# Kernel tuning notes

Hardware: AMD Instinct MI355X
Metric: run time of the kernel (lower is better)

The kernel has to match this reference:

```python
import jax, jax.numpy as jnp
import numpy as np

B, IN, OUT = 8192, 4096, 4096

def setup_inputs() -> dict:
    key = jax.random.key(0)
    ks = jax.random.split(key, 7)
    # sigma params initialized near -3 as in the torch module
    return {
        "x": jax.random.normal(ks[0], (B, IN), dtype=jnp.float32),
        "weight_mu": 0.1 * jax.random.normal(ks[1], (OUT, IN), dtype=jnp.float32),
        "weight_sigma": -3.0 + 0.1 * jax.random.normal(ks[2], (OUT, IN), dtype=jnp.float32),
        "bias_mu": 0.1 * jax.random.normal(ks[3], (OUT,), dtype=jnp.float32),
        "bias_sigma": -3.0 + 0.1 * jax.random.normal(ks[4], (OUT,), dtype=jnp.float32),
        "eps_w": jax.random.normal(ks[5], (OUT, IN), dtype=jnp.float32),
        "eps_b": jax.random.normal(ks[6], (OUT,), dtype=jnp.float32),
    }

def reference(x, weight_mu, weight_sigma, bias_mu, bias_sigma, eps_w, eps_b):
    # Reparameterized sample: w = mu + exp(sigma) * eps
    weight = weight_mu + jnp.exp(weight_sigma) * eps_w          # [OUT, IN]
    bias = bias_mu + jnp.exp(bias_sigma) * eps_b                # [OUT]
    out = jnp.einsum('bi,oi->bo', x, weight) + bias             # [B, OUT]
    # KL(q || N(0,1)); note log(var) == 2*sigma
    weight_var = jnp.exp(2.0 * weight_sigma)
    bias_var = jnp.exp(2.0 * bias_sigma)
    kl_w = -0.5 * jnp.sum(1.0 + 2.0 * weight_sigma - weight_mu ** 2 - weight_var)
    kl_b = -0.5 * jnp.sum(1.0 + 2.0 * bias_sigma - bias_mu ** 2 - bias_var)
    return out, kl_w + kl_b
```

## Files before the change

kernel.cpp:

```cpp
#include <hip/hip_runtime.h>

#define MDIM 8192
#define NDIM 4096
#define KDIM 4096
#define BK 32

typedef unsigned short u16;
typedef __attribute__((ext_vector_type(8))) short short8;
typedef __attribute__((ext_vector_type(4))) float f32x4;

__device__ __forceinline__ u16 f2b(float f) {
  unsigned u = __float_as_uint(f);
  u += 0x7FFFu + ((u >> 16) & 1u);
  return (u16)(u >> 16);
}
__device__ __forceinline__ unsigned pk2(float a, float b) {
  return (unsigned)f2b(a) | ((unsigned)f2b(b) << 16);
}

__device__ __forceinline__ void async16(const u16* g, u16* l) {
  __builtin_amdgcn_global_load_lds(
      (const __attribute__((address_space(1))) unsigned*)g,
      (__attribute__((address_space(3))) unsigned*)l, 16, 0, 0);
}

__global__ __launch_bounds__(256) void k_prep(const float4* __restrict__ wmu,
                                              const float4* __restrict__ wsg,
                                              const float4* __restrict__ wep,
                                              uint4* __restrict__ wb,
                                              const float4* __restrict__ x,
                                              uint4* __restrict__ xb,
                                              float* __restrict__ partials) {
  const int bx = blockIdx.x;
  if (bx < 8192) {
    const int i = bx * 256 + (int)threadIdx.x;
    float part = 0.f;
    uint4 o;
    {
      float4 m = wmu[2 * i], s = wsg[2 * i], e = wep[2 * i];
      float e0 = __expf(s.x), e1 = __expf(s.y), e2 = __expf(s.z), e3 = __expf(s.w);
      o.x = pk2(m.x + e0 * e.x, m.y + e1 * e.y);
      o.y = pk2(m.z + e2 * e.z, m.w + e3 * e.w);
      part += (1.f + 2.f * s.x - m.x * m.x - e0 * e0)
            + (1.f + 2.f * s.y - m.y * m.y - e1 * e1)
            + (1.f + 2.f * s.z - m.z * m.z - e2 * e2)
            + (1.f + 2.f * s.w - m.w * m.w - e3 * e3);
    }
    {
      float4 m = wmu[2 * i + 1], s = wsg[2 * i + 1], e = wep[2 * i + 1];
      float e0 = __expf(s.x), e1 = __expf(s.y), e2 = __expf(s.z), e3 = __expf(s.w);
      o.z = pk2(m.x + e0 * e.x, m.y + e1 * e.y);
      o.w = pk2(m.z + e2 * e.z, m.w + e3 * e.w);
      part += (1.f + 2.f * s.x - m.x * m.x - e0 * e0)
            + (1.f + 2.f * s.y - m.y * m.y - e1 * e1)
            + (1.f + 2.f * s.z - m.z * m.z - e2 * e2)
            + (1.f + 2.f * s.w - m.w * m.w - e3 * e3);
    }
    wb[i] = o;
    for (int off = 32; off; off >>= 1) part += __shfl_down(part, off, 64);
    __shared__ float red[4];
    const int lane = threadIdx.x & 63, wv = threadIdx.x >> 6;
    if (lane == 0) red[wv] = part;
    __syncthreads();
    if (threadIdx.x == 0)
      partials[bx] = red[0] + red[1] + red[2] + red[3];
  } else {
    const int i0 = (bx - 8192) * 256 + (int)threadIdx.x;
#pragma unroll
    for (int c = 0; c < 2; ++c) {
      const int i = i0 + c * (8192 * 256);
      float4 a = x[2 * i], b = x[2 * i + 1];
      uint4 o;
      o.x = pk2(a.x, a.y); o.y = pk2(a.z, a.w);
      o.z = pk2(b.x, b.y); o.w = pk2(b.z, b.w);
      xb[i] = o;
    }
  }
}

__global__ __launch_bounds__(1024) void k_bias(const float* __restrict__ bmu,
                                               const float* __restrict__ bsg,
                                               const float* __restrict__ bep,
                                               float* __restrict__ bias,
                                               const float* __restrict__ partials,
                                               int nPart,
                                               float* __restrict__ klOut) {
  float part = 0.f;
  for (int i = threadIdx.x; i < NDIM; i += 1024) {
    float s = bsg[i], m = bmu[i];
    float es = __expf(s);
    bias[i] = m + es * bep[i];
    part += 1.f + 2.f * s - m * m - es * es;
  }
  for (int i = threadIdx.x; i < nPart; i += 1024) part += partials[i];
  for (int off = 32; off; off >>= 1) part += __shfl_down(part, off, 64);
  __shared__ float red[16];
  const int lane = threadIdx.x & 63, wv = threadIdx.x >> 6;
  if (lane == 0) red[wv] = part;
  __syncthreads();
  if (threadIdx.x == 0) {
    float s = 0.f;
#pragma unroll
    for (int w = 0; w < 16; ++w) s += red[w];
    *klOut = -0.5f * s;
  }
}

__global__ __launch_bounds__(256) void k_gemm(const u16* __restrict__ A,
                                              const u16* __restrict__ B,
                                              const float* __restrict__ bias,
                                              float* __restrict__ C) {
  __shared__ u16 sA[128 * BK];
  __shared__ u16 sB[128 * BK];
  const int t = threadIdx.x;
  const int wave = t >> 6, lane = t & 63;

  const int lin = blockIdx.x;
  const int tile = lin >> 8, within = lin & 255;
  const int tm = within & 15, tn = within >> 4;
  const int sm = tile & 3, sn = tile >> 2;
  const int bm = (sm * 16 + tm) * 128;
  const int bn = (sn * 16 + tn) * 128;

  const int wm = (wave >> 1) * 64;
  const int wn = (wave & 1) * 64;

  const int srow = lane >> 2;
  const int scol = (lane & 3) * 8;
  const u16* gA0 = A + (size_t)(bm + wave * 32 + srow) * KDIM + scol;
  const u16* gA1 = gA0 + (size_t)16 * KDIM;
  const u16* gB0 = B + (size_t)(bn + wave * 32 + srow) * KDIM + scol;
  const u16* gB1 = gB0 + (size_t)16 * KDIM;
  u16* lA0 = &sA[(wave * 32) * BK];
  u16* lA1 = &sA[(wave * 32 + 16) * BK];
  u16* lB0 = &sB[(wave * 32) * BK];
  u16* lB1 = &sB[(wave * 32 + 16) * BK];

  const int fr = lane & 15;
  const int fg = lane >> 4;

  f32x4 acc[4][4] = {};

  for (int k0 = 0; k0 < KDIM; k0 += BK) {
    async16(gA0 + k0, lA0);
    async16(gA1 + k0, lA1);
    async16(gB0 + k0, lB0);
    async16(gB1 + k0, lB1);
    __syncthreads();

    short8 af[4], bf[4];
#pragma unroll
    for (int i = 0; i < 4; ++i) {
      af[i] = *(const short8*)&sA[(wm + i * 16 + fr) * BK + fg * 8];
      bf[i] = *(const short8*)&sB[(wn + i * 16 + fr) * BK + fg * 8];
    }
#pragma unroll
    for (int i = 0; i < 4; ++i)
#pragma unroll
      for (int j = 0; j < 4; ++j)
        acc[i][j] = __builtin_amdgcn_mfma_f32_16x16x32_bf16(af[i], bf[j],
                                                            acc[i][j], 0, 0, 0);
    __syncthreads();
  }

#pragma unroll
  for (int j = 0; j < 4; ++j) {
    const int gn = bn + wn + j * 16 + fr;
    const float bv = bias[gn];
#pragma unroll
    for (int i = 0; i < 4; ++i) {
      const int gm0 = bm + wm + i * 16 + fg * 4;
      float* Cp = C + (size_t)gm0 * NDIM + gn;
#pragma unroll
      for (int r = 0; r < 4; ++r)
        Cp[(size_t)r * NDIM] = acc[i][j][r] + bv;
    }
  }
}

extern "C" void kernel_launch(void* const* d_in, const int* in_sizes, int n_in,
                              void* d_out, int out_size, void* d_ws, size_t ws_size,
                              hipStream_t stream) {
  const float* x    = (const float*)d_in[0];
  const float* wmu  = (const float*)d_in[1];
  const float* wsig = (const float*)d_in[2];
  const float* bmu  = (const float*)d_in[3];
  const float* bsig = (const float*)d_in[4];
  const float* ew   = (const float*)d_in[5];
  const float* eb   = (const float*)d_in[6];
  float* out = (float*)d_out;

  char* ws = (char*)d_ws;
  u16*   xb       = (u16*)ws;
  u16*   wb       = (u16*)(ws + 67108864);
  float* bias     = (float*)(ws + 100663296);
  float* partials = (float*)(ws + 100679680);

  k_prep<<<16384, 256, 0, stream>>>((const float4*)wmu, (const float4*)wsig,
                                    (const float4*)ew, (uint4*)wb,
                                    (const float4*)x, (uint4*)xb, partials);
  k_bias<<<1, 1024, 0, stream>>>(bmu, bsig, eb, bias, partials, 8192,
                                 out + (size_t)MDIM * NDIM);
  k_gemm<<<2048, 256, 0, stream>>>(xb, wb, bias, out);
}
```

Before: 672.1 us.

## Rewrite GEMM as 256x256 tile with multi-buffered async LDS pipeline

Replaces the 128x128, 256-thread GEMM, which loads and computes in lockstep, with a 256x256 tile per 512-thread block. LDS is split into double-buffered halves, and global-to-LDS async loads are issued several sub-stages ahead of the MFMA phases. Waits use explicit vmcnt/lgkmcnt plus barriers, and MFMA priority is raised through setprio. The goal is to hide global memory latency and raise arithmetic intensity per loaded byte. In exchange it uses much more LDS and registers (128 accumulators per thread), drops the grouped tile ordering for L2 reuse, and relies on delicate hand-placed barrier and waitcnt ordering.

```diff
diff --git a/kernel.cpp b/kernel.cpp
--- a/kernel.cpp
+++ b/kernel.cpp
@@ -3,7 +3,6 @@
 #define MDIM 8192
 #define NDIM 4096
 #define KDIM 4096
-#define BK 32
 
 typedef unsigned short u16;
 typedef __attribute__((ext_vector_type(8))) short short8;
@@ -106,74 +105,98 @@
   }
 }
 
-__global__ __launch_bounds__(256) void k_gemm(const u16* __restrict__ A,
-                                              const u16* __restrict__ B,
-                                              const float* __restrict__ bias,
-                                              float* __restrict__ C) {
-  __shared__ u16 sA[128 * BK];
-  __shared__ u16 sB[128 * BK];
-  const int t = threadIdx.x;
-  const int wave = t >> 6, lane = t & 63;
-
-  const int lin = blockIdx.x;
-  const int tile = lin >> 8, within = lin & 255;
-  const int tm = within & 15, tn = within >> 4;
-  const int sm = tile & 3, sn = tile >> 2;
-  const int bm = (sm * 16 + tm) * 128;
-  const int bn = (sn * 16 + tn) * 128;
-
-  const int wm = (wave >> 1) * 64;
-  const int wn = (wave & 1) * 64;
-
-  const int srow = lane >> 2;
-  const int scol = (lane & 3) * 8;
-  const u16* gA0 = A + (size_t)(bm + wave * 32 + srow) * KDIM + scol;
-  const u16* gA1 = gA0 + (size_t)16 * KDIM;
-  const u16* gB0 = B + (size_t)(bn + wave * 32 + srow) * KDIM + scol;
-  const u16* gB1 = gB0 + (size_t)16 * KDIM;
-  u16* lA0 = &sA[(wave * 32) * BK];
-  u16* lA1 = &sA[(wave * 32 + 16) * BK];
-  u16* lB0 = &sB[(wave * 32) * BK];
-  u16* lB1 = &sB[(wave * 32 + 16) * BK];
-
+__global__ __launch_bounds__(512, 2) void k_gemm(const u16* __restrict__ A,
+                                                 const u16* __restrict__ B,
+                                                 const float* __restrict__ bias,
+                                                 float* __restrict__ C) {
+  __shared__ u16 sA[2][2][8192];
+  __shared__ u16 sB[2][2][8192];
+
+  const int tid = threadIdx.x;
+  const int wave = tid >> 6, lane = tid & 63;
   const int fr = lane & 15;
   const int fg = lane >> 4;
-
-  f32x4 acc[4][4] = {};
-
-  for (int k0 = 0; k0 < KDIM; k0 += BK) {
-    async16(gA0 + k0, lA0);
-    async16(gA1 + k0, lA1);
-    async16(gB0 + k0, lB0);
-    async16(gB1 + k0, lB1);
-    __syncthreads();
-
-    short8 af[4], bf[4];
-#pragma unroll
-    for (int i = 0; i < 4; ++i) {
-      af[i] = *(const short8*)&sA[(wm + i * 16 + fr) * BK + fg * 8];
-      bf[i] = *(const short8*)&sB[(wn + i * 16 + fr) * BK + fg * 8];
-    }
-#pragma unroll
-    for (int i = 0; i < 4; ++i)
-#pragma unroll
-      for (int j = 0; j < 4; ++j)
-        acc[i][j] = __builtin_amdgcn_mfma_f32_16x16x32_bf16(af[i], bf[j],
-                                                            acc[i][j], 0, 0, 0);
-    __syncthreads();
-  }
-
-#pragma unroll
-  for (int j = 0; j < 4; ++j) {
-    const int gn = bn + wn + j * 16 + fr;
+  const int wm128 = (wave >> 2) * 128;
+  const int wn64  = (wave & 3) * 64;
+  const int w512  = wave << 9;
+
+  const int bm = (blockIdx.x & 31) * 256;
+  const int bn = (blockIdx.x >> 5) * 256;
+
+  const u16* gA = A + (size_t)(bm + (tid >> 2)) * KDIM + (tid & 3) * 8;
+  const u16* gB = B + (size_t)(bn + (tid >> 2)) * KDIM + (tid & 3) * 8;
+
+#define STG(g, larr, ks)                                                     \
+  do {                                                                       \
+    async16((g) + (ks), &(larr)[0] + w512);                                  \
+    async16((g) + (size_t)128 * KDIM + (ks), &(larr)[0] + 4096 + w512);      \
+  } while (0)
+
+  f32x4 acc[8][4] = {};
+
+  STG(gA, sA[0][0], 0);
+  STG(gB, sB[0][0], 0);
+  STG(gA, sA[0][1], 32);
+  STG(gB, sB[0][1], 32);
+  STG(gA, sA[1][0], 64);
+  STG(gB, sB[1][0], 64);
+  asm volatile("s_waitcnt vmcnt(4)" ::: "memory");
+  __builtin_amdgcn_s_barrier();
+
+#define PHASE(BUF, H, QM, STAGE_STMT, TILE_END)                               \
+  {                                                                           \
+    short8 af[4], bf[4];                                                      \
+    _Pragma("unroll") for (int x = 0; x < 4; ++x) {                           \
+      af[x] = *(const short8*)&sA[BUF][H][(wm128 + (QM)*64 + x*16 + fr)*32 + fg*8]; \
+      bf[x] = *(const short8*)&sB[BUF][H][(wn64 + x*16 + fr)*32 + fg*8];      \
+    }                                                                         \
+    STAGE_STMT;                                                               \
+    __builtin_amdgcn_s_barrier();                                             \
+    asm volatile("s_waitcnt lgkmcnt(0)" ::: "memory");                        \
+    __builtin_amdgcn_sched_barrier(0);                                        \
+    __builtin_amdgcn_s_setprio(1);                                            \
+    _Pragma("unroll") for (int x = 0; x < 4; ++x)                             \
+      _Pragma("unroll") for (int y = 0; y < 4; ++y)                           \
+        acc[(QM)*4 + x][y] = __builtin_amdgcn_mfma_f32_16x16x32_bf16(         \
+            af[x], bf[y], acc[(QM)*4 + x][y], 0, 0, 0);                       \
+    __builtin_amdgcn_s_setprio(0);                                            \
+    if (TILE_END) asm volatile("s_waitcnt vmcnt(4)" ::: "memory");            \
+    __builtin_amdgcn_s_barrier();                                             \
+  }
+
+  for (int i = 0; i < 32; ++i) {
+    const int t = 2 * i;
+    int s1 = t + 1; if (s1 > 63) s1 = 63;
+    int s2 = t + 2; if (s2 > 63) s2 = 63;
+    int s3 = t + 3; if (s3 > 63) s3 = 63;
+    const int k1  = s1 * 64 + 32;
+    const int k2a = s2 * 64;
+    const int k2b = s2 * 64 + 32;
+    const int k3  = s3 * 64;
+
+    PHASE(0, 0, 0, STG(gA, sA[1][1], k1),  false)
+    PHASE(0, 0, 1, STG(gB, sB[1][1], k1),  false)
+    PHASE(0, 1, 0, STG(gA, sA[0][0], k2a), false)
+    PHASE(0, 1, 1, STG(gB, sB[0][0], k2a), true)
+    PHASE(1, 0, 0, STG(gA, sA[0][1], k2b), false)
+    PHASE(1, 0, 1, STG(gB, sB[0][1], k2b), false)
+    PHASE(1, 1, 0, STG(gA, sA[1][0], k3),  false)
+    PHASE(1, 1, 1, STG(gB, sB[1][0], k3),  true)
+  }
+#undef PHASE
+#undef STG
+
+#pragma unroll
+  for (int y = 0; y < 4; ++y) {
+    const int gn = bn + wn64 + y * 16 + fr;
     const float bv = bias[gn];
 #pragma unroll
-    for (int i = 0; i < 4; ++i) {
-      const int gm0 = bm + wm + i * 16 + fg * 4;
+    for (int x = 0; x < 8; ++x) {
+      const int gm0 = bm + wm128 + x * 16 + fg * 4;
       float* Cp = C + (size_t)gm0 * NDIM + gn;
 #pragma unroll
       for (int r = 0; r < 4; ++r)
-        Cp[(size_t)r * NDIM] = acc[i][j][r] + bv;
+        Cp[(size_t)r * NDIM] = acc[x][y][r] + bv;
     }
   }
 }
@@ -201,5 +224,5 @@
                                     (const float4*)x, (uint4*)xb, partials);
   k_bias<<<1, 1024, 0, stream>>>(bmu, bsig, eb, bias, partials, 8192,
                                  out + (size_t)MDIM * NDIM);
-  k_gemm<<<2048, 256, 0, stream>>>(xb, wb, bias, out);
-}
+  k_gemm<<<512, 512, 0, stream>>>(xb, wb, bias, out);
+}
```

Result: faster. 650.5 us (-3.2%).
